# Kernel optimization log

Hardware: AMD Instinct MI355X
Metric: run time of the kernel (lower is better)

## Reference

```python
import jax, jax.numpy as jnp
import numpy as np

B, S, D, H = 4, 4096, 2048, 16
DH = D // H
SCALE = float(np.sqrt(DH))


def setup_inputs() -> dict:
    key = jax.random.key(0)
    ks = jax.random.split(key, 11)
    std = 1.0 / np.sqrt(D)
    inp = {
        "query": jax.random.normal(ks[0], (B, S, D), jnp.float32),
        "key": jax.random.normal(ks[1], (B, S, D), jnp.float32),
        "value": jax.random.normal(ks[2], (B, S, D), jnp.float32),
        "Wq": jax.random.normal(ks[3], (D, D), jnp.float32) * std,
        "bq": jax.random.normal(ks[4], (D,), jnp.float32) * std,
        "Wk": jax.random.normal(ks[5], (D, D), jnp.float32) * std,
        "bk": jax.random.normal(ks[6], (D,), jnp.float32) * std,
        "Wv": jax.random.normal(ks[7], (D, D), jnp.float32) * std,
        "bv": jax.random.normal(ks[8], (D,), jnp.float32) * std,
        "Wo": jax.random.normal(ks[9], (D, D), jnp.float32) * std,
        "bo": jax.random.normal(ks[10], (D,), jnp.float32) * std,
    }
    return inp


def reference(query, key, value, Wq, bq, Wk, bk, Wv, bv, Wo, bo):
    # Linear projections (torch nn.Linear: x @ W^T + b)
    Q = query @ Wq.T + bq          # [B,S,D]
    K = key @ Wk.T + bk
    V = value @ Wv.T + bv
    Q = Q.reshape(B, S, H, DH)
    K = K.reshape(B, S, H, DH)
    V = V.reshape(B, S, H, DH)
    # NOTE: original torch code does NOT transpose heads to dim 1, so the
    # matmul contracts over head-dim pairs at each position: scores [B,S,H,H]
    scores = jnp.einsum('bsid,bsjd->bsij', Q, K) / SCALE
    attention = jax.nn.softmax(scores, axis=-1)   # softmax over heads (faithful)
    x = jnp.einsum('bsij,bsjd->bsid', attention, V)  # [B,S,H,DH]
    # permute(0,2,1,3) -> [B,H,S,DH], then view(B,-1,D) -> [B,S,D]
    x = jnp.transpose(x, (0, 2, 1, 3)).reshape(B, S, D)
    out = x @ Wo.T + bo
    return out, attention
```

## Files before the change

### kernel.cpp

```cpp
#include <hip/hip_runtime.h>


#define DEV __device__ __forceinline__

using short8  = __attribute__((ext_vector_type(8))) short;
using ushort8 = __attribute__((ext_vector_type(8))) unsigned short;
using f32x4   = __attribute__((ext_vector_type(4))) float;
using u16x8   = __attribute__((ext_vector_type(8))) unsigned short;

constexpr int BATCH = 4, SEQ = 4096, DIM = 2048;
constexpr int GM = BATCH * SEQ;
constexpr int GN = DIM, GK = DIM;

DEV unsigned short f2bf(float f) {
  unsigned int u = __builtin_bit_cast(unsigned int, f);
  u += 0x7FFFu + ((u >> 16) & 1u);
  return (unsigned short)(u >> 16);
}
DEV float bf2f(unsigned short h) {
  unsigned int u = ((unsigned int)h) << 16;
  return __builtin_bit_cast(float, u);
}

DEV void gload16(const void* g, void* l) {
  __builtin_amdgcn_global_load_lds(
      (const __attribute__((address_space(1))) void*)g,
      (__attribute__((address_space(3))) void*)l, 16, 0, 0);
}

#define BAR    __builtin_amdgcn_s_barrier()
#define LGKM0  asm volatile("s_waitcnt lgkmcnt(0)" ::: "memory")
#define VMC(N) asm volatile("s_waitcnt vmcnt(" #N ")" ::: "memory")
#define SCHED0 __builtin_amdgcn_sched_barrier(0)
#define PRIO1  __builtin_amdgcn_s_setprio(1)
#define PRIO0  __builtin_amdgcn_s_setprio(0)
#define MFMA16(a, b, c) __builtin_amdgcn_mfma_f32_16x16x32_bf16(a, b, c, 0, 0, 0)

__global__ void cvt_f32_bf16(const float* __restrict__ src,
                             unsigned short* __restrict__ dst, int n) {
  int i = (blockIdx.x * blockDim.x + threadIdx.x) * 4;
  if (i >= n) return;
  f32x4 f = *(const f32x4*)(src + i);
  ushort4 o;
  o.x = f2bf(f[0]); o.y = f2bf(f[1]); o.z = f2bf(f[2]); o.w = f2bf(f[3]);
  *(ushort4*)(dst + i) = o;
}

template <bool OUTF32>
__global__ __launch_bounds__(512, 2)
void gemm256(const unsigned short* __restrict__ Ap,
             const unsigned short* __restrict__ Bp,
             const float* __restrict__ bias, void* __restrict__ Cp) {
  constexpr int BK = 64, KT = GK / BK;
  __shared__ unsigned short As[2][256 * BK];
  __shared__ unsigned short Bs[2][256 * BK];

  const int tid  = threadIdx.x;
  const int lane = tid & 63;
  const int wv   = tid >> 6;
  const int wm   = wv >> 2, wn = wv & 3;

  int bid = (int)blockIdx.x;
  const int xcd = bid & 7, rr = bid >> 3;
  const int gg = rr >> 5, jj = rr & 31;
  const int mt = xcd * 8 + gg * 4 + (jj & 3);
  const int nt = jj >> 2;
  const int bm0 = mt * 256, bn0 = nt * 256;

  const int dst0 = tid * 16;
  int offA[4], offB[4];
#pragma unroll
  for (int r = 0; r < 4; ++r) {
    int d = dst0 + r * 8192;
    int s = d ^ (((d >> 7) & 7) << 4);
    int row = s >> 7, col = (s & 127) >> 1;
    offA[r] = (bm0 + row) * GK + col;
    offB[r] = (bn0 + row) * GK + col;
  }

  const int r16 = lane & 15, kb = (lane >> 4) * 16;
  const int arow = wm * 128 + r16;
  const int brow = wn * 64 + r16;

  f32x4 acc[8][4] = {};
  short8 af[4][2], bl[2][2], bh[2][2];

  auto stA = [&](int buf, int kt, int r) {
    gload16(Ap + (size_t)offA[r] + (size_t)kt * BK,
            (char*)&As[buf][0] + (dst0 + r * 8192));
  };
  auto stB = [&](int buf, int kt, int r) {
    gload16(Bp + (size_t)offB[r] + (size_t)kt * BK,
            (char*)&Bs[buf][0] + (dst0 + r * 8192));
  };
  auto ldf = [&](const unsigned short* base, int row, int ks) -> short8 {
    int a = (row * 128 + ks * 64 + kb) ^ ((row & 7) << 4);
    return *(const short8*)((const char*)base + a);
  };

#pragma unroll
  for (int r = 0; r < 4; ++r) stA(0, 0, r);
#pragma unroll
  for (int r = 0; r < 4; ++r) stB(0, 0, r);
#pragma unroll
  for (int r = 0; r < 4; ++r) stA(1, 1, r);
  VMC(4);
  BAR;
#pragma unroll
  for (int m = 0; m < 4; ++m) {
    af[m][0] = ldf(&As[0][0], arow + m * 16, 0);
    af[m][1] = ldf(&As[0][0], arow + m * 16, 1);
  }
#pragma unroll
  for (int n = 0; n < 2; ++n) {
    bl[n][0] = ldf(&Bs[0][0], brow + n * 16, 0);
    bl[n][1] = ldf(&Bs[0][0], brow + n * 16, 1);
  }

  for (int kt = 0; kt < KT; ++kt) {
    const int cb = kt & 1, nb = cb ^ 1;
    const unsigned short* Ab = &As[cb][0];
    const unsigned short* Bb = &Bs[cb][0];
    const unsigned short* An = &As[nb][0];
    const unsigned short* Bn = &Bs[nb][0];
    const bool m1 = (kt + 1 < KT), m2 = (kt + 2 < KT);

    if (m1) { stB(nb, kt + 1, 0); stB(nb, kt + 1, 1); }
    LGKM0; SCHED0;
    PRIO1;
#pragma unroll
    for (int m = 0; m < 4; ++m)
#pragma unroll
      for (int n = 0; n < 2; ++n) {
        acc[m][n] = MFMA16(af[m][0], bl[n][0], acc[m][n]);
        acc[m][n] = MFMA16(af[m][1], bl[n][1], acc[m][n]);
      }
#pragma unroll
    for (int n = 0; n < 2; ++n) {
      bh[n][0] = ldf(Bb, brow + 32 + n * 16, 0);
      bh[n][1] = ldf(Bb, brow + 32 + n * 16, 1);
    }
    PRIO0; SCHED0;

    if (m1) { stB(nb, kt + 1, 2); stB(nb, kt + 1, 3); }
    LGKM0; SCHED0;
    PRIO1;
#pragma unroll
    for (int m = 0; m < 4; ++m)
#pragma unroll
      for (int n = 0; n < 2; ++n) {
        acc[m][2 + n] = MFMA16(af[m][0], bh[n][0], acc[m][2 + n]);
        acc[m][2 + n] = MFMA16(af[m][1], bh[n][1], acc[m][2 + n]);
      }
#pragma unroll
    for (int m = 0; m < 4; ++m) {
      af[m][0] = ldf(Ab, arow + 64 + m * 16, 0);
      af[m][1] = ldf(Ab, arow + 64 + m * 16, 1);
    }
    PRIO0; SCHED0;
    BAR;

    if (m2) { stA(cb, kt + 2, 0); stA(cb, kt + 2, 2); }
    LGKM0; SCHED0;
    PRIO1;
#pragma unroll
    for (int m = 0; m < 4; ++m)
#pragma unroll
      for (int n = 0; n < 2; ++n) {
        acc[4 + m][2 + n] = MFMA16(af[m][0], bh[n][0], acc[4 + m][2 + n]);
        acc[4 + m][2 + n] = MFMA16(af[m][1], bh[n][1], acc[4 + m][2 + n]);
      }
    PRIO0; SCHED0;
    BAR;

    if (m2) { stA(cb, kt + 2, 1); stA(cb, kt + 2, 3); }
    if (m2) { VMC(4); } else { VMC(0); }
    SCHED0;
    BAR;
    PRIO1;
#pragma unroll
    for (int m = 0; m < 4; ++m)
#pragma unroll
      for (int n = 0; n < 2; ++n) {
        acc[4 + m][n] = MFMA16(af[m][0], bl[n][0], acc[4 + m][n]);
        acc[4 + m][n] = MFMA16(af[m][1], bl[n][1], acc[4 + m][n]);
      }
    if (m1) {
#pragma unroll
      for (int m = 0; m < 4; ++m) {
        af[m][0] = ldf(An, arow + m * 16, 0);
        af[m][1] = ldf(An, arow + m * 16, 1);
      }
#pragma unroll
      for (int n = 0; n < 2; ++n) {
        bl[n][0] = ldf(Bn, brow + n * 16, 0);
        bl[n][1] = ldf(Bn, brow + n * 16, 1);
      }
    }
    PRIO0; SCHED0;
  }

  float bs[4];
#pragma unroll
  for (int n = 0; n < 4; ++n) bs[n] = bias[bn0 + wn * 64 + n * 16 + r16];
  const int rb = (lane >> 4) * 4;
#pragma unroll
  for (int m = 0; m < 8; ++m)
#pragma unroll
    for (int i = 0; i < 4; ++i) {
      const size_t row = (size_t)bm0 + wm * 128 + m * 16 + rb + i;
#pragma unroll
      for (int n = 0; n < 4; ++n) {
        const int col = bn0 + wn * 64 + n * 16 + r16;
        float v = acc[m][n][i] + bs[n];
        if constexpr (OUTF32)
          ((float*)Cp)[row * GN + col] = v;
        else
          ((unsigned short*)Cp)[row * GN + col] = f2bf(v);
      }
    }
}

__global__ __launch_bounds__(256)
void attn_kernel(const unsigned short* __restrict__ Qb,
                 const unsigned short* __restrict__ Kb,
                 const unsigned short* __restrict__ Vb,
                 float* __restrict__ attnOut,
                 unsigned short* __restrict__ X2) {
  __shared__ float qf[16 * 128];
  __shared__ float kf[16 * 132];
  __shared__ float vf[16 * 128];
  __shared__ float sc[256];

  const int t = threadIdx.x;
  const int p = blockIdx.x;
  const size_t rowoff = (size_t)p * DIM;

  {
    const int e = t * 8;
    u16x8 qv = *(const u16x8*)(Qb + rowoff + e);
    u16x8 kv = *(const u16x8*)(Kb + rowoff + e);
    u16x8 vv = *(const u16x8*)(Vb + rowoff + e);
    const int r = t >> 4, c = (t & 15) * 8;
#pragma unroll
    for (int j = 0; j < 8; ++j) qf[r * 128 + c + j] = bf2f(qv[j]);
#pragma unroll
    for (int j = 0; j < 8; ++j) kf[r * 132 + c + j] = bf2f(kv[j]);
#pragma unroll
    for (int j = 0; j < 8; ++j) vf[r * 128 + c + j] = bf2f(vv[j]);
  }
  __syncthreads();

  const int i = t >> 4, j = t & 15;
  float s = 0.f;
#pragma unroll
  for (int d4 = 0; d4 < 32; ++d4) {
    f32x4 q4 = *(const f32x4*)&qf[i * 128 + d4 * 4];
    f32x4 k4 = *(const f32x4*)&kf[j * 132 + d4 * 4];
    s = fmaf(q4[0], k4[0], fmaf(q4[1], k4[1], fmaf(q4[2], k4[2], fmaf(q4[3], k4[3], s))));
  }
  s *= 0.08838834764831845f;

  float mx = s;
#pragma unroll
  for (int off = 8; off; off >>= 1) mx = fmaxf(mx, __shfl_xor(mx, off, 16));
  float ex = __expf(s - mx);
  float sum = ex;
#pragma unroll
  for (int off = 8; off; off >>= 1) sum += __shfl_xor(sum, off, 16);
  float a = ex / sum;

  attnOut[(size_t)p * 256 + t] = a;
  sc[t] = a;
  __syncthreads();

  const int dh0 = j * 8;
  float o[8] = {};
#pragma unroll
  for (int jjq = 0; jjq < 16; ++jjq) {
    float aij = sc[i * 16 + jjq];
#pragma unroll
    for (int e2 = 0; e2 < 8; ++e2)
      o[e2] = fmaf(aij, vf[jjq * 128 + dh0 + e2], o[e2]);
  }
  const int b = p >> 12, spos = p & 4095;
  const int row = i * 256 + (spos >> 4);
  const int col = ((spos & 15) << 7) + dh0;
  ushort8 pk;
#pragma unroll
  for (int e2 = 0; e2 < 8; ++e2) pk[e2] = f2bf(o[e2]);
  *(ushort8*)(X2 + (size_t)b * (SEQ * DIM) + (size_t)row * DIM + col) = pk;
}

extern "C" void kernel_launch(void* const* d_in, const int* in_sizes, int n_in,
                              void* d_out, int out_size, void* d_ws,
                              size_t ws_size, hipStream_t stream) {
  const float* q  = (const float*)d_in[0];
  const float* k  = (const float*)d_in[1];
  const float* v  = (const float*)d_in[2];
  const float* Wq = (const float*)d_in[3];
  const float* bq = (const float*)d_in[4];
  const float* Wk = (const float*)d_in[5];
  const float* bk = (const float*)d_in[6];
  const float* Wv = (const float*)d_in[7];
  const float* bv = (const float*)d_in[8];
  const float* Wo = (const float*)d_in[9];
  const float* bo = (const float*)d_in[10];

  const size_t NE = (size_t)GM * GK;
  const size_t WE = (size_t)GK * GN;

  unsigned short* ws16 = (unsigned short*)d_ws;
  unsigned short* Wq_b = ws16;
  unsigned short* Wk_b = Wq_b + WE;
  unsigned short* Wv_b = Wk_b + WE;
  unsigned short* Wo_b = Wv_b + WE;
  unsigned short* Qb   = Wo_b + WE;
  unsigned short* Kb   = Qb + NE;
  unsigned short* Vb   = Kb + NE;
  unsigned short* X2   = Vb + NE;
  unsigned short* Qin  = X2 + NE;
  unsigned short* Kin  = Qin + NE;
  unsigned short* Vin  = Kin + NE;

  float* outMain = (float*)d_out;
  float* attnOut = outMain + (size_t)GM * GN;

  cvt_f32_bf16<<<WE / 1024, 256, 0, stream>>>(Wq, Wq_b, (int)WE);
  cvt_f32_bf16<<<WE / 1024, 256, 0, stream>>>(Wk, Wk_b, (int)WE);
  cvt_f32_bf16<<<WE / 1024, 256, 0, stream>>>(Wv, Wv_b, (int)WE);
  cvt_f32_bf16<<<WE / 1024, 256, 0, stream>>>(Wo, Wo_b, (int)WE);

  cvt_f32_bf16<<<NE / 1024, 256, 0, stream>>>(q, Qin, (int)NE);
  cvt_f32_bf16<<<NE / 1024, 256, 0, stream>>>(k, Kin, (int)NE);
  cvt_f32_bf16<<<NE / 1024, 256, 0, stream>>>(v, Vin, (int)NE);

  constexpr int G256 = (GM / 256) * (GN / 256);

  gemm256<false><<<G256, 512, 0, stream>>>(Qin, Wq_b, bq, Qb);
  gemm256<false><<<G256, 512, 0, stream>>>(Kin, Wk_b, bk, Kb);
  gemm256<false><<<G256, 512, 0, stream>>>(Vin, Wv_b, bv, Vb);

  attn_kernel<<<GM, 256, 0, stream>>>(Qb, Kb, Vb, attnOut, X2);

  gemm256<true><<<G256, 512, 0, stream>>>(X2, Wo_b, bo, outMain);
}
```

Before: 822.2 us.

## Restructure GEMM pipeline into half-tile LDS buffers with per-half prefetch

Splits the A and B shared-memory tiles into two 128-row halves and reorganizes the main loop. A halves for the next k-step and B halves two steps ahead are issued one at a time between the four MFMA quadrants. Fragment loads for the current tile now happen at the start of each iteration rather than being prefetched at the end of the previous one. More barriers are added, one after each quadrant, which raises synchronization cost in exchange for finer-grained overlap of global-to-LDS loads with compute.

```diff
diff --git a/kernel.cpp b/kernel.cpp
--- a/kernel.cpp
+++ b/kernel.cpp
@@ -30,6 +30,7 @@
 
 #define BAR    __builtin_amdgcn_s_barrier()
 #define LGKM0  asm volatile("s_waitcnt lgkmcnt(0)" ::: "memory")
+#define LGKM8  asm volatile("s_waitcnt lgkmcnt(8)" ::: "memory")
 #define VMC(N) asm volatile("s_waitcnt vmcnt(" #N ")" ::: "memory")
 #define SCHED0 __builtin_amdgcn_sched_barrier(0)
 #define PRIO1  __builtin_amdgcn_s_setprio(1)
@@ -52,8 +53,8 @@
              const unsigned short* __restrict__ Bp,
              const float* __restrict__ bias, void* __restrict__ Cp) {
   constexpr int BK = 64, KT = GK / BK;
-  __shared__ unsigned short As[2][256 * BK];
-  __shared__ unsigned short Bs[2][256 * BK];
+  __shared__ unsigned short As[2][2][128 * 64];
+  __shared__ unsigned short Bs[2][2][128 * 64];
 
   const int tid  = threadIdx.x;
   const int lane = tid & 63;
@@ -67,66 +68,67 @@
   const int nt = jj >> 2;
   const int bm0 = mt * 256, bn0 = nt * 256;
 
-  const int dst0 = tid * 16;
-  int offA[4], offB[4];
-#pragma unroll
-  for (int r = 0; r < 4; ++r) {
-    int d = dst0 + r * 8192;
+  int dst_[2];
+  size_t offA_[2][2], offB_[2][2];
+#pragma unroll
+  for (int r = 0; r < 2; ++r) {
+    int d = tid * 16 + r * 8192;
     int s = d ^ (((d >> 7) & 7) << 4);
     int row = s >> 7, col = (s & 127) >> 1;
-    offA[r] = (bm0 + row) * GK + col;
-    offB[r] = (bn0 + row) * GK + col;
+    dst_[r] = d;
+#pragma unroll
+    for (int h = 0; h < 2; ++h) {
+      offA_[h][r] = (size_t)(bm0 + h * 128 + row) * GK + col;
+      offB_[h][r] = (size_t)(bn0 + h * 128 + row) * GK + col;
+    }
   }
 
   const int r16 = lane & 15, kb = (lane >> 4) * 16;
-  const int arow = wm * 128 + r16;
-  const int brow = wn * 64 + r16;
+  const int bhalf = wn >> 1;
+  const int brow0 = (wn & 1) * 64 + r16;
 
   f32x4 acc[8][4] = {};
   short8 af[4][2], bl[2][2], bh[2][2];
 
-  auto stA = [&](int buf, int kt, int r) {
-    gload16(Ap + (size_t)offA[r] + (size_t)kt * BK,
-            (char*)&As[buf][0] + (dst0 + r * 8192));
+  auto stA = [&](int buf, int h, int T) {
+#pragma unroll
+    for (int r = 0; r < 2; ++r)
+      gload16(Ap + offA_[h][r] + (size_t)T * BK, (char*)&As[buf][h][0] + dst_[r]);
   };
-  auto stB = [&](int buf, int kt, int r) {
-    gload16(Bp + (size_t)offB[r] + (size_t)kt * BK,
-            (char*)&Bs[buf][0] + (dst0 + r * 8192));
+  auto stB = [&](int buf, int h, int T) {
+#pragma unroll
+    for (int r = 0; r < 2; ++r)
+      gload16(Bp + offB_[h][r] + (size_t)T * BK, (char*)&Bs[buf][h][0] + dst_[r]);
   };
-  auto ldf = [&](const unsigned short* base, int row, int ks) -> short8 {
-    int a = (row * 128 + ks * 64 + kb) ^ ((row & 7) << 4);
+  auto ldf = [&](const unsigned short* base, int rowh, int ks) -> short8 {
+    int a = (rowh * 128 + ks * 64 + kb) ^ ((rowh & 7) << 4);
     return *(const short8*)((const char*)base + a);
   };
 
-#pragma unroll
-  for (int r = 0; r < 4; ++r) stA(0, 0, r);
-#pragma unroll
-  for (int r = 0; r < 4; ++r) stB(0, 0, r);
-#pragma unroll
-  for (int r = 0; r < 4; ++r) stA(1, 1, r);
+  stA(0, 0, 0); stA(0, 1, 0);
+  stB(0, 0, 0); stB(0, 1, 0);
+  stB(1, 0, 1); stB(1, 1, 1);
   VMC(4);
   BAR;
-#pragma unroll
-  for (int m = 0; m < 4; ++m) {
-    af[m][0] = ldf(&As[0][0], arow + m * 16, 0);
-    af[m][1] = ldf(&As[0][0], arow + m * 16, 1);
-  }
-#pragma unroll
-  for (int n = 0; n < 2; ++n) {
-    bl[n][0] = ldf(&Bs[0][0], brow + n * 16, 0);
-    bl[n][1] = ldf(&Bs[0][0], brow + n * 16, 1);
-  }
-
-  for (int kt = 0; kt < KT; ++kt) {
-    const int cb = kt & 1, nb = cb ^ 1;
-    const unsigned short* Ab = &As[cb][0];
-    const unsigned short* Bb = &Bs[cb][0];
-    const unsigned short* An = &As[nb][0];
-    const unsigned short* Bn = &Bs[nb][0];
-    const bool m1 = (kt + 1 < KT), m2 = (kt + 2 < KT);
-
-    if (m1) { stB(nb, kt + 1, 0); stB(nb, kt + 1, 1); }
-    LGKM0; SCHED0;
+
+  for (int T = 0; T < KT; ++T) {
+    const int bb = T & 1;
+    const unsigned short* Abase = &As[bb][wm][0];
+    const unsigned short* Bbase = &Bs[bb][bhalf][0];
+    const bool m1 = (T + 1 < KT), m2 = (T + 2 < KT);
+
+#pragma unroll
+    for (int m = 0; m < 4; ++m) {
+      af[m][0] = ldf(Abase, m * 16 + r16, 0);
+      af[m][1] = ldf(Abase, m * 16 + r16, 1);
+    }
+#pragma unroll
+    for (int n = 0; n < 2; ++n) {
+      bl[n][0] = ldf(Bbase, brow0 + n * 16, 0);
+      bl[n][1] = ldf(Bbase, brow0 + n * 16, 1);
+    }
+    if (m1) stA(bb ^ 1, 0, T + 1);
+    LGKM8; SCHED0; BAR; LGKM0; SCHED0;
     PRIO1;
 #pragma unroll
     for (int m = 0; m < 4; ++m)
@@ -135,15 +137,15 @@
         acc[m][n] = MFMA16(af[m][0], bl[n][0], acc[m][n]);
         acc[m][n] = MFMA16(af[m][1], bl[n][1], acc[m][n]);
       }
+    PRIO0; SCHED0; BAR;
+
 #pragma unroll
     for (int n = 0; n < 2; ++n) {
-      bh[n][0] = ldf(Bb, brow + 32 + n * 16, 0);
-      bh[n][1] = ldf(Bb, brow + 32 + n * 16, 1);
-    }
-    PRIO0; SCHED0;
-
-    if (m1) { stB(nb, kt + 1, 2); stB(nb, kt + 1, 3); }
-    LGKM0; SCHED0;
+      bh[n][0] = ldf(Bbase, brow0 + 32 + n * 16, 0);
+      bh[n][1] = ldf(Bbase, brow0 + 32 + n * 16, 1);
+    }
+    if (m1) stA(bb ^ 1, 1, T + 1);
+    SCHED0; BAR; LGKM0; SCHED0;
     PRIO1;
 #pragma unroll
     for (int m = 0; m < 4; ++m)
@@ -152,16 +154,15 @@
         acc[m][2 + n] = MFMA16(af[m][0], bh[n][0], acc[m][2 + n]);
         acc[m][2 + n] = MFMA16(af[m][1], bh[n][1], acc[m][2 + n]);
       }
+    PRIO0; SCHED0; BAR;
+
 #pragma unroll
     for (int m = 0; m < 4; ++m) {
-      af[m][0] = ldf(Ab, arow + 64 + m * 16, 0);
-      af[m][1] = ldf(Ab, arow + 64 + m * 16, 1);
-    }
-    PRIO0; SCHED0;
-    BAR;
-
-    if (m2) { stA(cb, kt + 2, 0); stA(cb, kt + 2, 2); }
-    LGKM0; SCHED0;
+      af[m][0] = ldf(Abase, 64 + m * 16 + r16, 0);
+      af[m][1] = ldf(Abase, 64 + m * 16 + r16, 1);
+    }
+    if (m2) stB(bb, 0, T + 2);
+    SCHED0; BAR; LGKM0; SCHED0;
     PRIO1;
 #pragma unroll
     for (int m = 0; m < 4; ++m)
@@ -170,13 +171,15 @@
         acc[4 + m][2 + n] = MFMA16(af[m][0], bh[n][0], acc[4 + m][2 + n]);
         acc[4 + m][2 + n] = MFMA16(af[m][1], bh[n][1], acc[4 + m][2 + n]);
       }
-    PRIO0; SCHED0;
-    BAR;
-
-    if (m2) { stA(cb, kt + 2, 1); stA(cb, kt + 2, 3); }
-    if (m2) { VMC(4); } else { VMC(0); }
-    SCHED0;
-    BAR;
+    PRIO0; SCHED0; BAR;
+
+    if (m2) {
+      stB(bb, 1, T + 2);
+      SCHED0; VMC(4);
+    } else {
+      SCHED0; VMC(0);
+    }
+    SCHED0; BAR;
     PRIO1;
 #pragma unroll
     for (int m = 0; m < 4; ++m)
@@ -185,19 +188,7 @@
         acc[4 + m][n] = MFMA16(af[m][0], bl[n][0], acc[4 + m][n]);
         acc[4 + m][n] = MFMA16(af[m][1], bl[n][1], acc[4 + m][n]);
       }
-    if (m1) {
-#pragma unroll
-      for (int m = 0; m < 4; ++m) {
-        af[m][0] = ldf(An, arow + m * 16, 0);
-        af[m][1] = ldf(An, arow + m * 16, 1);
-      }
-#pragma unroll
-      for (int n = 0; n < 2; ++n) {
-        bl[n][0] = ldf(Bn, brow + n * 16, 0);
-        bl[n][1] = ldf(Bn, brow + n * 16, 1);
-      }
-    }
-    PRIO0; SCHED0;
+    PRIO0; SCHED0; BAR;
   }
 
   float bs[4];
```

After: 857.4 us. +4.3%, slower.
